# Performance work log

Measured on AMD Instinct MI355X. Metric: run time of the kernel, lower is better.

The kernel has to match this reference:

```python
import jax, jax.numpy as jnp
import numpy as np

L, D, H, KV, HD, FF = 5, 1024, 16, 8, 128, 3072
B, T = 1, 2048
G = H // KV
EPS = 1e-6
ROPE_THETA = 1e6


def setup_inputs() -> dict:
    key = jax.random.key(0)
    ks = jax.random.split(key, 8)
    s = 0.02  # init scale keeps activations stable across 5 layers
    return {
        "inputs_embeds": jax.random.normal(ks[0], (B, T, D), jnp.float32),
        "ln1_w": jnp.ones((L, D), jnp.float32),
        "q_w": jax.random.normal(ks[1], (L, H * HD, D), jnp.float32) * s,
        "k_w": jax.random.normal(ks[2], (L, KV * HD, D), jnp.float32) * s,
        "v_w": jax.random.normal(ks[3], (L, KV * HD, D), jnp.float32) * s,
        "qn_w": jnp.ones((L, HD), jnp.float32),
        "kn_w": jnp.ones((L, HD), jnp.float32),
        "o_w": jax.random.normal(ks[4], (L, D, H * HD), jnp.float32) * s,
        "ln2_w": jnp.ones((L, D), jnp.float32),
        "gate_w": jax.random.normal(ks[5], (L, FF, D), jnp.float32) * s,
        "up_w": jax.random.normal(ks[6], (L, FF, D), jnp.float32) * s,
        "down_w": jax.random.normal(ks[7], (L, D, FF), jnp.float32) * s,
        "norm_w": jnp.ones((D,), jnp.float32),
    }


def _rms(x, w):
    # Qwen3 RMSNorm: fp32 variance, scale by weight
    var = jnp.mean(jnp.square(x.astype(jnp.float32)), axis=-1, keepdims=True)
    return (x * jax.lax.rsqrt(var + EPS).astype(x.dtype)) * w


def _rope_tables():
    inv_freq = 1.0 / (ROPE_THETA ** (jnp.arange(0, HD, 2, dtype=jnp.float32) / HD))
    pos = jnp.arange(T, dtype=jnp.float32)
    freqs = pos[:, None] * inv_freq[None, :]          # (T, HD/2)
    emb = jnp.concatenate([freqs, freqs], axis=-1)    # (T, HD)
    return jnp.cos(emb)[None, None], jnp.sin(emb)[None, None]  # (1,1,T,HD)


def _apply_rope(x, cos, sin):
    # x: (B, nh, T, HD); rotate_half = cat(-x2, x1)
    x1, x2 = x[..., : HD // 2], x[..., HD // 2 :]
    return x * cos + jnp.concatenate([-x2, x1], axis=-1) * sin


def reference(inputs_embeds, ln1_w, q_w, k_w, v_w, qn_w, kn_w, o_w, ln2_w,
              gate_w, up_w, down_w, norm_w):
    cos, sin = _rope_tables()
    mask = jnp.triu(jnp.full((T, T), jnp.finfo(jnp.float32).min, jnp.float32), 1)
    scale = HD ** -0.5
    h = inputs_embeds
    keys, vals = [], []
    for i in range(L):
        x = _rms(h, ln1_w[i])
        q = jnp.einsum('btd,ed->bte', x, q_w[i]).reshape(B, T, H, HD)
        k = jnp.einsum('btd,ed->bte', x, k_w[i]).reshape(B, T, KV, HD)
        v = jnp.einsum('btd,ed->bte', x, v_w[i]).reshape(B, T, KV, HD)
        q = _rms(q, qn_w[i]).transpose(0, 2, 1, 3)   # (B,H,T,HD)
        k = _rms(k, kn_w[i]).transpose(0, 2, 1, 3)   # (B,KV,T,HD)
        v = v.transpose(0, 2, 1, 3)                   # (B,KV,T,HD)
        q = _apply_rope(q, cos, sin)
        k = _apply_rope(k, cos, sin)
        keys.append(k)
        vals.append(v)
        # GQA: group Q heads per KV head instead of materializing repeat_kv
        qg = q.reshape(B, KV, G, T, HD)
        scores = jnp.einsum('bkgtd,bksd->bkgts', qg, k) * scale + mask
        attn = jax.nn.softmax(scores.astype(jnp.float32), axis=-1).astype(q.dtype)
        out = jnp.einsum('bkgts,bksd->bkgtd', attn, v)
        out = out.reshape(B, H, T, HD).transpose(0, 2, 1, 3).reshape(B, T, H * HD)
        h = h + jnp.einsum('bte,de->btd', out, o_w[i])
        y = _rms(h, ln2_w[i])
        g = jax.nn.silu(jnp.einsum('btd,fd->btf', y, gate_w[i]))
        u = jnp.einsum('btd,fd->btf', y, up_w[i])
        h = h + jnp.einsum('btf,df->btd', g * u, down_w[i])
    hs = _rms(h, norm_w)
    return hs, jnp.stack(keys), jnp.stack(vals)
```

## Files before the change

### kernel.cpp

```cpp
#include <hip/hip_runtime.h>
#include <hip/hip_bf16.h>
#include <math.h>

#define LAYERS 5
#define DMODEL 1024
#define NH 16
#define NKV 8
#define HDIM 128
#define FFD 3072
#define SEQ 2048
#define RMS_EPS 1e-6f
#define SC2 0.12753292444440332f
#define NEGINF (-1e30f)

typedef __attribute__((ext_vector_type(8))) short bf16x8;
typedef __attribute__((ext_vector_type(4))) float f32x4;
typedef __attribute__((ext_vector_type(4))) unsigned short u16x4;

__device__ __forceinline__ unsigned short f2bf(float x) {
    unsigned int u = __float_as_uint(x);
    u = (u + 0x7fffu + ((u >> 16) & 1u)) >> 16;
    return (unsigned short)u;
}
__device__ __forceinline__ float bf2f(unsigned short b) {
    return __uint_as_float(((unsigned int)b) << 16);
}
__device__ __forceinline__ void fsplit(float x, unsigned short &h, unsigned short &l) {
    h = f2bf(x);
    l = f2bf(x - bf2f(h));
}

__global__ void rope_init_k(float* __restrict__ cosT, float* __restrict__ sinT) {
    int t = blockIdx.x;
    int j = threadIdx.x;
    double inv = pow(1.0e6, -((double)j) / 64.0);
    float angf = (float)t * (float)inv;
    double ang = (double)angf;
    cosT[t * 64 + j] = (float)cos(ang);
    sinT[t * 64 + j] = (float)sin(ang);
}

template <bool SPLIT>
__global__ __launch_bounds__(256) void rms_k(const float* __restrict__ in,
                                             const float* __restrict__ w,
                                             float* __restrict__ outf,
                                             unsigned short* __restrict__ oh,
                                             unsigned short* __restrict__ ol) {
    __shared__ float red[4];
    const int row = blockIdx.x;
    const int t = threadIdx.x;
    const float* p = in + (size_t)row * DMODEL;
    float4 v = *(const float4*)(p + t * 4);
    float ss = v.x * v.x + v.y * v.y + v.z * v.z + v.w * v.w;
#pragma unroll
    for (int off = 32; off >= 1; off >>= 1) ss += __shfl_xor(ss, off);
    if ((t & 63) == 0) red[t >> 6] = ss;
    __syncthreads();
    float tot = red[0] + red[1] + red[2] + red[3];
    float scale = rsqrtf(tot * (1.0f / DMODEL) + RMS_EPS);
    float4 w4 = *(const float4*)(w + t * 4);
    float o0 = v.x * scale * w4.x;
    float o1 = v.y * scale * w4.y;
    float o2 = v.z * scale * w4.z;
    float o3 = v.w * scale * w4.w;
    if (SPLIT) {
        unsigned short h0, h1, h2, h3, l0, l1, l2, l3;
        fsplit(o0, h0, l0); fsplit(o1, h1, l1); fsplit(o2, h2, l2); fsplit(o3, h3, l3);
        u16x4 hh = {h0, h1, h2, h3};
        u16x4 ll = {l0, l1, l2, l3};
        *(u16x4*)(oh + (size_t)row * DMODEL + t * 4) = hh;
        *(u16x4*)(ol + (size_t)row * DMODEL + t * 4) = ll;
    } else {
        float4 o = {o0, o1, o2, o3};
        *(float4*)(outf + (size_t)row * DMODEL + t * 4) = o;
    }
}

__global__ __launch_bounds__(256) void convert_w_k(const float* __restrict__ src,
                                                   unsigned short* __restrict__ hi,
                                                   unsigned short* __restrict__ lo,
                                                   int n4) {
    int i = blockIdx.x * 256 + threadIdx.x;
    if (i >= n4) return;
    float4 v = ((const float4*)src)[i];
    unsigned short h0, h1, h2, h3, l0, l1, l2, l3;
    fsplit(v.x, h0, l0); fsplit(v.y, h1, l1); fsplit(v.z, h2, l2); fsplit(v.w, h3, l3);
    u16x4 hh = {h0, h1, h2, h3};
    u16x4 ll = {l0, l1, l2, l3};
    ((u16x4*)hi)[i] = hh;
    ((u16x4*)lo)[i] = ll;
}

template <int BM, bool ACC>
__global__ __launch_bounds__(256, 2) void gemm_sp(
    const unsigned short* __restrict__ Ah, const unsigned short* __restrict__ Al,
    const unsigned short* __restrict__ Bh, const unsigned short* __restrict__ Bl,
    float* __restrict__ C, int N, int K, int actsplit) {
    constexpr int WM = (BM == 128) ? 2 : 1;
    constexpr int WN = 4 / WM;
    constexpr int WNS = 128 / WN;
    constexpr int NF = WNS / 16;
    constexpr int AUNITS = BM * 4;
    constexpr int AISS = BM / 64;
    __shared__ __align__(16) char lds[(AUNITS * 2 + 1024) * 16];
    char* ldsAh = lds;
    char* ldsAl = lds + AUNITS * 16;
    char* ldsBh = lds + AUNITS * 32;
    char* ldsBl = lds + AUNITS * 32 + 8192;

    const int tid = threadIdx.x;
    const int lane = tid & 63, wave = tid >> 6;
    const int wm = (BM == 128) ? (wave >> 1) : 0;
    const int wn = (BM == 128) ? (wave & 1) : wave;
    const int lr = lane & 15, lg = lane >> 4;
    const int m0 = blockIdx.y * BM, n0 = blockIdx.x * 128;

    f32x4 zero = {0.f, 0.f, 0.f, 0.f};
    f32x4 acc[4][NF];
#pragma unroll
    for (int m = 0; m < 4; ++m)
#pragma unroll
        for (int n = 0; n < NF; ++n) acc[m][n] = zero;

    const int swz = (lr >> 1) & 3;

    for (int k0 = 0; k0 < K; k0 += 32) {
#pragma unroll
        for (int i = 0; i < AISS; ++i) {
            const int u = i * 256 + wave * 64 + lane;
            const int row = u >> 2, cs = u & 3;
            const int c = cs ^ ((row >> 1) & 3);
            const size_t goff = (size_t)(m0 + row) * K + k0 + c * 8;
            const int lbase = (i * 256 + wave * 64) * 16;
            __builtin_amdgcn_global_load_lds(
                (const __attribute__((address_space(1))) void*)(Ah + goff),
                (__attribute__((address_space(3))) void*)(ldsAh + lbase), 16, 0, 0);
            __builtin_amdgcn_global_load_lds(
                (const __attribute__((address_space(1))) void*)(Al + goff),
                (__attribute__((address_space(3))) void*)(ldsAl + lbase), 16, 0, 0);
        }
#pragma unroll
        for (int i = 0; i < 2; ++i) {
            const int u = i * 256 + wave * 64 + lane;
            const int row = u >> 2, cs = u & 3;
            const int c = cs ^ ((row >> 1) & 3);
            const size_t goff = (size_t)(n0 + row) * K + k0 + c * 8;
            const int lbase = (i * 256 + wave * 64) * 16;
            __builtin_amdgcn_global_load_lds(
                (const __attribute__((address_space(1))) void*)(Bh + goff),
                (__attribute__((address_space(3))) void*)(ldsBh + lbase), 16, 0, 0);
            __builtin_amdgcn_global_load_lds(
                (const __attribute__((address_space(1))) void*)(Bl + goff),
                (__attribute__((address_space(3))) void*)(ldsBl + lbase), 16, 0, 0);
        }
        __syncthreads();
        bf16x8 fAh[4], fAl[4], fBh[NF], fBl[NF];
#pragma unroll
        for (int m = 0; m < 4; ++m) {
            const int row = wm * 64 + m * 16 + lr;
            const int u = row * 4 + (lg ^ swz);
            fAh[m] = *(const bf16x8*)(ldsAh + u * 16);
            fAl[m] = *(const bf16x8*)(ldsAl + u * 16);
        }
#pragma unroll
        for (int n = 0; n < NF; ++n) {
            const int row = wn * WNS + n * 16 + lr;
            const int u = row * 4 + (lg ^ swz);
            fBh[n] = *(const bf16x8*)(ldsBh + u * 16);
            fBl[n] = *(const bf16x8*)(ldsBl + u * 16);
        }
#pragma unroll
        for (int m = 0; m < 4; ++m)
#pragma unroll
            for (int n = 0; n < NF; ++n) {
                acc[m][n] = __builtin_amdgcn_mfma_f32_16x16x32_bf16(fAl[m], fBh[n], acc[m][n], 0, 0, 0);
                acc[m][n] = __builtin_amdgcn_mfma_f32_16x16x32_bf16(fAh[m], fBl[n], acc[m][n], 0, 0, 0);
                acc[m][n] = __builtin_amdgcn_mfma_f32_16x16x32_bf16(fAh[m], fBh[n], acc[m][n], 0, 0, 0);
            }
        __syncthreads();
    }
#pragma unroll
    for (int m = 0; m < 4; ++m) {
        const int row = m0 + wm * 64 + m * 16 + lg * 4;
#pragma unroll
        for (int n = 0; n < NF; ++n) {
            const int col = n0 + wn * WNS + n * 16 + lr;
            const bool act = col < actsplit;
            float* cp = C + (size_t)row * N + col;
#pragma unroll
            for (int j = 0; j < 4; ++j) {
                float v = acc[m][n][j];
                if (act) v = v / (1.0f + expf(-v));
                if (ACC) cp[(size_t)j * N] += v;
                else cp[(size_t)j * N] = v;
            }
        }
    }
}

__global__ __launch_bounds__(256) void qkv_post_k(
    const float* __restrict__ qbuf, const float* __restrict__ kvbuf,
    const float* __restrict__ qn, const float* __restrict__ kn,
    const float* __restrict__ cosT, const float* __restrict__ sinT,
    unsigned short* __restrict__ qb16, float* __restrict__ keys,
    unsigned short* __restrict__ kb16, float* __restrict__ vals) {
    const int r = blockIdx.x * 4 + (threadIdx.x >> 6);
    const int lane = threadIdx.x & 63;
    const int t = r >> 5, c = r & 31;
    if (c >= 24) {
        const int vh = c - 24;
        const float* src = kvbuf + (size_t)t * 2048 + 1024 + vh * 128;
        float* dst = vals + ((size_t)vh * SEQ + t) * 128;
        dst[lane] = src[lane];
        dst[lane + 64] = src[lane + 64];
        return;
    }
    const float* src;
    const float* nw;
    if (c < 16) { src = qbuf + (size_t)t * 2048 + c * 128; nw = qn; }
    else        { src = kvbuf + (size_t)t * 2048 + (c - 16) * 128; nw = kn; }
    float x1 = src[lane], x2 = src[lane + 64];
    float ss = x1 * x1 + x2 * x2;
#pragma unroll
    for (int off = 32; off >= 1; off >>= 1) ss += __shfl_xor(ss, off);
    float scale = rsqrtf(ss * (1.0f / HDIM) + RMS_EPS);
    float xn1 = x1 * scale * nw[lane];
    float xn2 = x2 * scale * nw[lane + 64];
    float cc = cosT[t * 64 + lane], sv = sinT[t * 64 + lane];
    float o1 = xn1 * cc - xn2 * sv;
    float o2 = xn2 * cc + xn1 * sv;
    if (c < 16) {
        unsigned short* dst = qb16 + ((size_t)c * SEQ + t) * 128;
        dst[lane] = f2bf(o1);
        dst[lane + 64] = f2bf(o2);
    } else {
        const int kh = c - 16;
        float* kd = keys + ((size_t)kh * SEQ + t) * 128;
        kd[lane] = o1;
        kd[lane + 64] = o2;
        unsigned short* kb = kb16 + ((size_t)kh * SEQ + t) * 128;
        kb[lane] = f2bf(o1);
        kb[lane + 64] = f2bf(o2);
    }
}

__global__ __launch_bounds__(256) void vtrans_k(const float* __restrict__ vals,
                                                unsigned short* __restrict__ vt) {
    __shared__ float tile[32][33];
    const int t0 = blockIdx.x * 32, d0 = blockIdx.y * 32, kvh = blockIdx.z;
    const int a = threadIdx.x >> 3, b4 = (threadIdx.x & 7) * 4;
    const float4 v = *(const float4*)(vals + ((size_t)kvh * SEQ + t0 + a) * 128 + d0 + b4);
    tile[a][b4] = v.x; tile[a][b4 + 1] = v.y; tile[a][b4 + 2] = v.z; tile[a][b4 + 3] = v.w;
    __syncthreads();
    u16x4 o = {f2bf(tile[b4][a]), f2bf(tile[b4 + 1][a]), f2bf(tile[b4 + 2][a]), f2bf(tile[b4 + 3][a])};
    *(u16x4*)(vt + ((size_t)kvh * HDIM + d0 + a) * SEQ + t0 + b4) = o;
}

__global__ __launch_bounds__(128, 1) void attn_k(
    const unsigned short* __restrict__ Qb, const unsigned short* __restrict__ Kb,
    const unsigned short* __restrict__ Vt,
    unsigned short* __restrict__ AOh, unsigned short* __restrict__ AOl) {
    __shared__ __align__(16) char lds[73728];
    const int tid = threadIdx.x;
    const int wave = tid >> 6, lane = tid & 63;
    const int lr = lane & 15, lg = lane >> 4;
    const int head = blockIdx.y, kvh = head >> 1;
    const int qtile = blockIdx.x;
    const int qw = qtile * 64 + wave * 32;
    char* Pw = lds + 65536 + wave * 4096;
    const size_t kbase = (size_t)kvh * SEQ;
    const size_t vtb = (size_t)kvh * HDIM;

    bf16x8 qf[2][4];
#pragma unroll
    for (int qg = 0; qg < 2; ++qg)
#pragma unroll
        for (int ds = 0; ds < 4; ++ds)
            qf[qg][ds] = *(const bf16x8*)(Qb + ((size_t)head * SEQ + qw + qg * 16 + lr) * 128 + ds * 32 + lg * 8);

    f32x4 zero = {0.f, 0.f, 0.f, 0.f};
    f32x4 oacc[2][8];
#pragma unroll
    for (int qg = 0; qg < 2; ++qg)
#pragma unroll
        for (int dg = 0; dg < 8; ++dg) oacc[qg][dg] = zero;
    float m_r[2] = {NEGINF, NEGINF};
    float l_r[2] = {0.f, 0.f};

    auto stage = [&](int k0, int b) {
        const int kOff = b ? 16384 : 0;
        const int vOff = b ? 49152 : 32768;
#pragma unroll
        for (int i = 0; i < 8; ++i) {
            const int L = (i * 2 + wave) * 64 + lane;
            const int row = L >> 4, u = L & 15;
            const unsigned short* src = Kb + (kbase + k0 + row) * 128 + ((u ^ (row & 7)) << 3);
            __builtin_amdgcn_global_load_lds(
                (const __attribute__((address_space(1))) void*)src,
                (__attribute__((address_space(3))) void*)(lds + kOff + ((i * 2 + wave) << 10)), 16, 0, 0);
        }
#pragma unroll
        for (int i = 0; i < 8; ++i) {
            const int L = (i * 2 + wave) * 64 + lane;
            const int row = L >> 3, u = L & 7;
            const unsigned short* src = Vt + (vtb + row) * 2048 + k0 + ((u ^ (row & 7)) << 3);
            __builtin_amdgcn_global_load_lds(
                (const __attribute__((address_space(1))) void*)src,
                (__attribute__((address_space(3))) void*)(lds + vOff + ((i * 2 + wave) << 10)), 16, 0, 0);
        }
    };

    const int nsteps = qtile + 1;
    stage(0, 0);
    for (int s = 0; s < nsteps; ++s) {
        const int cur = s & 1;
        const int k0 = s * 64;
        if (s + 1 < nsteps) {
            stage((s + 1) * 64, cur ^ 1);
            asm volatile("s_waitcnt vmcnt(16)" ::: "memory");
        } else {
            asm volatile("s_waitcnt vmcnt(0)" ::: "memory");
        }
        __builtin_amdgcn_s_barrier();

        const int kOff = cur ? 16384 : 0;
        const int vOff = cur ? 49152 : 32768;
        f32x4 S[4][2];
#pragma unroll
        for (int kg = 0; kg < 4; ++kg) { S[kg][0] = zero; S[kg][1] = zero; }
        __builtin_amdgcn_s_setprio(1);
#pragma unroll
        for (int ds = 0; ds < 4; ++ds) {
#pragma unroll
            for (int kg = 0; kg < 4; ++kg) {
                const int krow = kg * 16 + lr;
                bf16x8 kf = *(const bf16x8*)(lds + kOff + ((krow * 16 + ((ds * 4 + lg) ^ (krow & 7))) << 4));
                S[kg][0] = __builtin_amdgcn_mfma_f32_16x16x32_bf16(kf, qf[0][ds], S[kg][0], 0, 0, 0);
                S[kg][1] = __builtin_amdgcn_mfma_f32_16x16x32_bf16(kf, qf[1][ds], S[kg][1], 0, 0, 0);
            }
        }
        __builtin_amdgcn_s_setprio(0);
        const bool diag = (s == qtile);
#pragma unroll
        for (int qg = 0; qg < 2; ++qg) {
            const int q = qw + qg * 16 + lr;
            float p[4][4];
            float mm = NEGINF;
#pragma unroll
            for (int kg = 0; kg < 4; ++kg)
#pragma unroll
                for (int j = 0; j < 4; ++j) {
                    float sv = S[kg][qg][j] * SC2;
                    if (diag) {
                        const int kk = k0 + kg * 16 + lg * 4 + j;
                        sv = (kk <= q) ? sv : NEGINF;
                    }
                    p[kg][j] = sv;
                    mm = fmaxf(mm, sv);
                }
            mm = fmaxf(mm, __shfl_xor(mm, 16));
            mm = fmaxf(mm, __shfl_xor(mm, 32));
            if (!__all(mm <= m_r[qg] + 11.5f)) {
                const float mnew = fmaxf(m_r[qg], mm);
                const float alpha = exp2f(m_r[qg] - mnew);
                l_r[qg] *= alpha;
#pragma unroll
                for (int dg = 0; dg < 8; ++dg) oacc[qg][dg] *= alpha;
                m_r[qg] = mnew;
            }
            float ps = 0.f;
            const int qloc = qg * 16 + lr;
#pragma unroll
            for (int kg = 0; kg < 4; ++kg) {
                u16x4 pw;
#pragma unroll
                for (int j = 0; j < 4; ++j) {
                    const float e = exp2f(p[kg][j] - m_r[qg]);
                    ps += e;
                    pw[j] = f2bf(e);
                }
                *(u16x4*)(Pw + ((qloc * 128 + kg * 32 + lg * 8) ^ ((lr & 7) << 4))) = pw;
            }
            ps += __shfl_xor(ps, 16);
            ps += __shfl_xor(ps, 32);
            l_r[qg] += ps;
        }
        asm volatile("s_waitcnt lgkmcnt(0)" ::: "memory");
        bf16x8 pf[2][2];
#pragma unroll
        for (int qg = 0; qg < 2; ++qg)
#pragma unroll
            for (int ks = 0; ks < 2; ++ks) {
                const int qloc = qg * 16 + lr;
                pf[qg][ks] = *(const bf16x8*)(Pw + ((qloc * 128 + ks * 64 + lg * 16) ^ ((lr & 7) << 4)));
            }
        __builtin_amdgcn_s_setprio(1);
#pragma unroll
        for (int dg = 0; dg < 8; ++dg) {
            const int drow = dg * 16 + lr;
#pragma unroll
            for (int ks = 0; ks < 2; ++ks) {
                bf16x8 vf = *(const bf16x8*)(lds + vOff + ((drow * 8 + ((ks * 4 + lg) ^ (drow & 7))) << 4));
                oacc[0][dg] = __builtin_amdgcn_mfma_f32_16x16x32_bf16(vf, pf[0][ks], oacc[0][dg], 0, 0, 0);
                oacc[1][dg] = __builtin_amdgcn_mfma_f32_16x16x32_bf16(vf, pf[1][ks], oacc[1][dg], 0, 0, 0);
            }
        }
        __builtin_amdgcn_s_setprio(0);
        __builtin_amdgcn_s_barrier();
    }

    const float inv0 = 1.0f / l_r[0];
    const float inv1 = 1.0f / l_r[1];
#pragma unroll
    for (int qg = 0; qg < 2; ++qg) {
        const float iv = qg ? inv1 : inv0;
        const int t = qw + qg * 16 + lr;
#pragma unroll
        for (int dg = 0; dg < 8; ++dg) {
            const int col = head * 128 + dg * 16 + lg * 4;
            float v0 = oacc[qg][dg][0] * iv, v1 = oacc[qg][dg][1] * iv;
            float v2 = oacc[qg][dg][2] * iv, v3 = oacc[qg][dg][3] * iv;
            unsigned short h0, h1, h2, h3, l0, l1, l2, l3;
            fsplit(v0, h0, l0); fsplit(v1, h1, l1); fsplit(v2, h2, l2); fsplit(v3, h3, l3);
            u16x4 hh = {h0, h1, h2, h3};
            u16x4 ll = {l0, l1, l2, l3};
            *(u16x4*)(AOh + (size_t)t * 2048 + col) = hh;
            *(u16x4*)(AOl + (size_t)t * 2048 + col) = ll;
        }
    }
}

__global__ __launch_bounds__(256) void mulsplit_k(const float* __restrict__ gu,
                                                  unsigned short* __restrict__ ph,
                                                  unsigned short* __restrict__ pl) {
    const int c4 = blockIdx.x * 256 + threadIdx.x;
    const int row = blockIdx.y;
    const float* base = gu + (size_t)row * 6144;
    float4 g = *(const float4*)(base + c4 * 4);
    float4 u = *(const float4*)(base + 3072 + c4 * 4);
    float p0 = g.x * u.x, p1 = g.y * u.y, p2 = g.z * u.z, p3 = g.w * u.w;
    unsigned short h0, h1, h2, h3, l0, l1, l2, l3;
    fsplit(p0, h0, l0); fsplit(p1, h1, l1); fsplit(p2, h2, l2); fsplit(p3, h3, l3);
    u16x4 hh = {h0, h1, h2, h3};
    u16x4 ll = {l0, l1, l2, l3};
    *(u16x4*)(ph + (size_t)row * 3072 + c4 * 4) = hh;
    *(u16x4*)(pl + (size_t)row * 3072 + c4 * 4) = ll;
}

extern "C" void kernel_launch(void* const* d_in, const int* in_sizes, int n_in,
                              void* d_out, int out_size, void* d_ws, size_t ws_size,
                              hipStream_t stream) {
    const float* emb = (const float*)d_in[0];
    const float* ln1 = (const float*)d_in[1];
    const float* qw  = (const float*)d_in[2];
    const float* kw  = (const float*)d_in[3];
    const float* vw  = (const float*)d_in[4];
    const float* qn  = (const float*)d_in[5];
    const float* kn  = (const float*)d_in[6];
    const float* ow  = (const float*)d_in[7];
    const float* ln2 = (const float*)d_in[8];
    const float* gw  = (const float*)d_in[9];
    const float* uw  = (const float*)d_in[10];
    const float* dw  = (const float*)d_in[11];
    const float* nw  = (const float*)d_in[12];

    float* out  = (float*)d_out;
    float* keys = out + (size_t)SEQ * DMODEL;
    float* vals = keys + (size_t)LAYERS * NKV * SEQ * HDIM;

    char* W = (char*)d_ws;
    float* h             = (float*)(W);
    unsigned short* xh   = (unsigned short*)(W + (8ull << 20));
    unsigned short* xl   = (unsigned short*)(W + (12ull << 20));
    float* qbuf          = (float*)(W + (16ull << 20));
    float* kvbuf         = (float*)(W + (32ull << 20));
    unsigned short* qb16 = (unsigned short*)(W + (48ull << 20));
    unsigned short* kb16 = (unsigned short*)(W + (56ull << 20));
    unsigned short* vt16 = (unsigned short*)(W + (60ull << 20));
    unsigned short* aoh  = (unsigned short*)(W + (64ull << 20));
    unsigned short* aol  = (unsigned short*)(W + (72ull << 20));
    float* gu            = (float*)(W + (16ull << 20));
    unsigned short* ph   = (unsigned short*)(W + (64ull << 20));
    unsigned short* pl   = (unsigned short*)(W + (76ull << 20));
    unsigned short* wh   = (unsigned short*)(W + (88ull << 20));
    unsigned short* wl   = (unsigned short*)(W + (100ull << 20));
    float* cosT          = (float*)(W + (112ull << 20));
    float* sinT          = cosT + SEQ * 64;

    hipMemcpyAsync(h, emb, sizeof(float) * SEQ * DMODEL, hipMemcpyDeviceToDevice, stream);
    rope_init_k<<<SEQ, 64, 0, stream>>>(cosT, sinT);

    for (int i = 0; i < LAYERS; ++i) {
        float* keys_i = keys + (size_t)i * NKV * SEQ * HDIM;
        float* vals_i = vals + (size_t)i * NKV * SEQ * HDIM;
        rms_k<true><<<SEQ, 256, 0, stream>>>(h, ln1 + (size_t)i * DMODEL, nullptr, xh, xl);
        convert_w_k<<<2048, 256, 0, stream>>>(qw + (size_t)i * 2097152, wh, wl, 524288);
        gemm_sp<128, false><<<dim3(16, 16), 256, 0, stream>>>(xh, xl, wh, wl, qbuf, 2048, 1024, 0);
        convert_w_k<<<1024, 256, 0, stream>>>(kw + (size_t)i * 1048576, wh, wl, 262144);
        convert_w_k<<<1024, 256, 0, stream>>>(vw + (size_t)i * 1048576, wh + 1048576, wl + 1048576, 262144);
        gemm_sp<128, false><<<dim3(16, 16), 256, 0, stream>>>(xh, xl, wh, wl, kvbuf, 2048, 1024, 0);
        qkv_post_k<<<SEQ * 32 / 4, 256, 0, stream>>>(qbuf, kvbuf, qn + (size_t)i * HDIM,
                                                     kn + (size_t)i * HDIM, cosT, sinT,
                                                     qb16, keys_i, kb16, vals_i);
        vtrans_k<<<dim3(SEQ / 32, HDIM / 32, NKV), 256, 0, stream>>>(vals_i, vt16);
        attn_k<<<dim3(SEQ / 64, NH), 128, 0, stream>>>(qb16, kb16, vt16, aoh, aol);
        convert_w_k<<<2048, 256, 0, stream>>>(ow + (size_t)i * 2097152, wh, wl, 524288);
        gemm_sp<64, true><<<dim3(8, 32), 256, 0, stream>>>(aoh, aol, wh, wl, h, 1024, 2048, 0);
        rms_k<true><<<SEQ, 256, 0, stream>>>(h, ln2 + (size_t)i * DMODEL, nullptr, xh, xl);
        convert_w_k<<<3072, 256, 0, stream>>>(gw + (size_t)i * 3145728, wh, wl, 786432);
        convert_w_k<<<3072, 256, 0, stream>>>(uw + (size_t)i * 3145728, wh + 3145728, wl + 3145728, 786432);
        gemm_sp<128, false><<<dim3(48, 16), 256, 0, stream>>>(xh, xl, wh, wl, gu, 6144, 1024, 3072);
        mulsplit_k<<<dim3(3, SEQ), 256, 0, stream>>>(gu, ph, pl);
        convert_w_k<<<3072, 256, 0, stream>>>(dw + (size_t)i * 3145728, wh, wl, 786432);
        gemm_sp<64, true><<<dim3(8, 32), 256, 0, stream>>>(ph, pl, wh, wl, h, 1024, 3072, 0);
    }
    rms_k<false><<<SEQ, 256, 0, stream>>>(h, nw, out, nullptr, nullptr);
}
```

Before: 2.751 ms.

## Double-buffer LDS in split-bf16 GEMM and add split-K for residual GEMMs

The split-precision GEMM now keeps two LDS stages, issuing global-to-LDS loads for the next K step before computing the current one. Explicit vmcnt waits and raw barriers replace __syncthreads, and MFMA sections are wrapped in s_setprio. The O-projection and down-projection GEMMs split K in two across blockIdx.z and accumulate into the residual with atomicAdd, doubling the block count for those 256-block launches. The costs are doubled LDS use per block, atomic traffic, and summation order that is no longer deterministic.

```diff
diff --git a/kernel.cpp b/kernel.cpp
--- a/kernel.cpp
+++ b/kernel.cpp
@@ -91,8 +91,8 @@
     ((u16x4*)lo)[i] = ll;
 }
 
-template <int BM, bool ACC>
-__global__ __launch_bounds__(256, 2) void gemm_sp(
+template <int BM, bool ACC, int SPLITK>
+__global__ __launch_bounds__(256, (BM == 64) ? 3 : 2) void gemm_sp(
     const unsigned short* __restrict__ Ah, const unsigned short* __restrict__ Al,
     const unsigned short* __restrict__ Bh, const unsigned short* __restrict__ Bl,
     float* __restrict__ C, int N, int K, int actsplit) {
@@ -102,11 +102,8 @@
     constexpr int NF = WNS / 16;
     constexpr int AUNITS = BM * 4;
     constexpr int AISS = BM / 64;
-    __shared__ __align__(16) char lds[(AUNITS * 2 + 1024) * 16];
-    char* ldsAh = lds;
-    char* ldsAl = lds + AUNITS * 16;
-    char* ldsBh = lds + AUNITS * 32;
-    char* ldsBl = lds + AUNITS * 32 + 8192;
+    constexpr int SBUF = (AUNITS * 2 + 1024) * 16;
+    __shared__ __align__(16) char lds[2 * SBUF];
 
     const int tid = threadIdx.x;
     const int lane = tid & 63, wave = tid >> 6;
@@ -114,6 +111,8 @@
     const int wn = (BM == 128) ? (wave & 1) : wave;
     const int lr = lane & 15, lg = lane >> 4;
     const int m0 = blockIdx.y * BM, n0 = blockIdx.x * 128;
+    const int Kc = K / SPLITK;
+    const int kbeg = (SPLITK > 1) ? blockIdx.z * Kc : 0;
 
     f32x4 zero = {0.f, 0.f, 0.f, 0.f};
     f32x4 acc[4][NF];
@@ -124,7 +123,11 @@
 
     const int swz = (lr >> 1) & 3;
 
-    for (int k0 = 0; k0 < K; k0 += 32) {
+    auto stage = [&](int k0, int b) {
+        char* ldsAh = lds + b * SBUF;
+        char* ldsAl = ldsAh + AUNITS * 16;
+        char* ldsBh = ldsAh + AUNITS * 32;
+        char* ldsBl = ldsBh + 8192;
 #pragma unroll
         for (int i = 0; i < AISS; ++i) {
             const int u = i * 256 + wave * 64 + lane;
@@ -153,7 +156,28 @@
                 (const __attribute__((address_space(1))) void*)(Bl + goff),
                 (__attribute__((address_space(3))) void*)(ldsBl + lbase), 16, 0, 0);
         }
-        __syncthreads();
+    };
+
+    const int nsteps = Kc / 32;
+    stage(kbeg, 0);
+    for (int s = 0; s < nsteps; ++s) {
+        const int cur = s & 1;
+        if (s + 1 < nsteps) {
+            stage(kbeg + (s + 1) * 32, cur ^ 1);
+            if constexpr (AISS == 2) {
+                asm volatile("s_waitcnt vmcnt(8)" ::: "memory");
+            } else {
+                asm volatile("s_waitcnt vmcnt(6)" ::: "memory");
+            }
+        } else {
+            asm volatile("s_waitcnt vmcnt(0)" ::: "memory");
+        }
+        __builtin_amdgcn_s_barrier();
+
+        char* ldsAh = lds + cur * SBUF;
+        char* ldsAl = ldsAh + AUNITS * 16;
+        char* ldsBh = ldsAh + AUNITS * 32;
+        char* ldsBl = ldsBh + 8192;
         bf16x8 fAh[4], fAl[4], fBh[NF], fBl[NF];
 #pragma unroll
         for (int m = 0; m < 4; ++m) {
@@ -169,6 +193,7 @@
             fBh[n] = *(const bf16x8*)(ldsBh + u * 16);
             fBl[n] = *(const bf16x8*)(ldsBl + u * 16);
         }
+        __builtin_amdgcn_s_setprio(1);
 #pragma unroll
         for (int m = 0; m < 4; ++m)
 #pragma unroll
@@ -177,7 +202,8 @@
                 acc[m][n] = __builtin_amdgcn_mfma_f32_16x16x32_bf16(fAh[m], fBl[n], acc[m][n], 0, 0, 0);
                 acc[m][n] = __builtin_amdgcn_mfma_f32_16x16x32_bf16(fAh[m], fBh[n], acc[m][n], 0, 0, 0);
             }
-        __syncthreads();
+        __builtin_amdgcn_s_setprio(0);
+        __builtin_amdgcn_s_barrier();
     }
 #pragma unroll
     for (int m = 0; m < 4; ++m) {
@@ -191,8 +217,12 @@
             for (int j = 0; j < 4; ++j) {
                 float v = acc[m][n][j];
                 if (act) v = v / (1.0f + expf(-v));
-                if (ACC) cp[(size_t)j * N] += v;
-                else cp[(size_t)j * N] = v;
+                if (ACC) {
+                    if (SPLITK > 1) atomicAdd(cp + (size_t)j * N, v);
+                    else cp[(size_t)j * N] += v;
+                } else {
+                    cp[(size_t)j * N] = v;
+                }
             }
         }
     }
@@ -495,24 +525,24 @@
         float* vals_i = vals + (size_t)i * NKV * SEQ * HDIM;
         rms_k<true><<<SEQ, 256, 0, stream>>>(h, ln1 + (size_t)i * DMODEL, nullptr, xh, xl);
         convert_w_k<<<2048, 256, 0, stream>>>(qw + (size_t)i * 2097152, wh, wl, 524288);
-        gemm_sp<128, false><<<dim3(16, 16), 256, 0, stream>>>(xh, xl, wh, wl, qbuf, 2048, 1024, 0);
+        gemm_sp<128, false, 1><<<dim3(16, 16), 256, 0, stream>>>(xh, xl, wh, wl, qbuf, 2048, 1024, 0);
         convert_w_k<<<1024, 256, 0, stream>>>(kw + (size_t)i * 1048576, wh, wl, 262144);
         convert_w_k<<<1024, 256, 0, stream>>>(vw + (size_t)i * 1048576, wh + 1048576, wl + 1048576, 262144);
-        gemm_sp<128, false><<<dim3(16, 16), 256, 0, stream>>>(xh, xl, wh, wl, kvbuf, 2048, 1024, 0);
+        gemm_sp<128, false, 1><<<dim3(16, 16), 256, 0, stream>>>(xh, xl, wh, wl, kvbuf, 2048, 1024, 0);
         qkv_post_k<<<SEQ * 32 / 4, 256, 0, stream>>>(qbuf, kvbuf, qn + (size_t)i * HDIM,
                                                      kn + (size_t)i * HDIM, cosT, sinT,
                                                      qb16, keys_i, kb16, vals_i);
         vtrans_k<<<dim3(SEQ / 32, HDIM / 32, NKV), 256, 0, stream>>>(vals_i, vt16);
         attn_k<<<dim3(SEQ / 64, NH), 128, 0, stream>>>(qb16, kb16, vt16, aoh, aol);
         convert_w_k<<<2048, 256, 0, stream>>>(ow + (size_t)i * 2097152, wh, wl, 524288);
-        gemm_sp<64, true><<<dim3(8, 32), 256, 0, stream>>>(aoh, aol, wh, wl, h, 1024, 2048, 0);
+        gemm_sp<64, true, 2><<<dim3(8, 32, 2), 256, 0, stream>>>(aoh, aol, wh, wl, h, 1024, 2048, 0);
         rms_k<true><<<SEQ, 256, 0, stream>>>(h, ln2 + (size_t)i * DMODEL, nullptr, xh, xl);
         convert_w_k<<<3072, 256, 0, stream>>>(gw + (size_t)i * 3145728, wh, wl, 786432);
         convert_w_k<<<3072, 256, 0, stream>>>(uw + (size_t)i * 3145728, wh + 3145728, wl + 3145728, 786432);
-        gemm_sp<128, false><<<dim3(48, 16), 256, 0, stream>>>(xh, xl, wh, wl, gu, 6144, 1024, 3072);
+        gemm_sp<128, false, 1><<<dim3(48, 16), 256, 0, stream>>>(xh, xl, wh, wl, gu, 6144, 1024, 3072);
         mulsplit_k<<<dim3(3, SEQ), 256, 0, stream>>>(gu, ph, pl);
         convert_w_k<<<3072, 256, 0, stream>>>(dw + (size_t)i * 3145728, wh, wl, 786432);
-        gemm_sp<64, true><<<dim3(8, 32), 256, 0, stream>>>(ph, pl, wh, wl, h, 1024, 3072, 0);
+        gemm_sp<64, true, 2><<<dim3(8, 32, 2), 256, 0, stream>>>(ph, pl, wh, wl, h, 1024, 3072, 0);
     }
     rms_k<false><<<SEQ, 256, 0, stream>>>(h, nw, out, nullptr, nullptr);
 }
```

Measured after the change: 2.241 ms. 18.5% less time.
